# Optimization experiments

Measured on AMD Instinct MI355X. Metric: run time of the kernel, lower is better.

The kernel has to match this reference:

```python
import jax, jax.numpy as jnp
import numpy as np

N = 100_000   # nodes
E = 1_600_000 # edges
G = 128       # graphs in batch
DIN, DOUT = 100, 200


def setup_inputs() -> dict:
    key = jax.random.key(0)
    ks = jax.random.split(key, 12)
    def lin_w(k, fan_in, fan_out):
        return (jax.random.normal(k, (fan_in, fan_out), jnp.float32) / np.sqrt(fan_in)).astype(jnp.float32)
    return {
        "x": jax.random.normal(ks[0], (N, DIN), jnp.float32),
        "edge_index": jax.random.randint(ks[1], (2, E), 0, N, dtype=jnp.int32),
        "batch": jnp.sort(jax.random.randint(ks[2], (N,), 0, G, dtype=jnp.int32)),
        "W1": lin_w(ks[3], DIN, DOUT),  "b1": jnp.zeros((DOUT,), jnp.float32),
        "Wc": lin_w(ks[4], DOUT, DOUT), "bc": jnp.zeros((DOUT,), jnp.float32),
        "W2": lin_w(ks[5], DOUT, DOUT), "b2": jnp.zeros((DOUT,), jnp.float32),
        "W3": lin_w(ks[6], DOUT, DOUT), "b3": jnp.zeros((DOUT,), jnp.float32),
        "Wcls": lin_w(ks[7], DOUT, 2),  "bcls": jnp.zeros((2,), jnp.float32),
    }


def gcn_conv(x, W, b, src, dst, n_nodes):
    """PyG GCNConv: D^{-1/2}(A+I)D^{-1/2} X W + b, symmetric norm with self-loops."""
    h = x @ W  # [N, Dout]
    # degree at targets including the self-loop (+1)
    deg = jax.ops.segment_sum(jnp.ones((src.shape[0],), x.dtype), dst, num_segments=n_nodes) + 1.0
    dinv = jax.lax.rsqrt(deg)  # [N]
    # gather -> normalize -> scatter-add (messages along edges)
    msg = h[src] * (dinv[src] * dinv[dst])[:, None]          # [E, Dout]
    agg = jax.ops.segment_sum(msg, dst, num_segments=n_nodes)  # [N, Dout]
    # self-loop contribution handled analytically: norm_ii = dinv[i]^2
    agg = agg + h * (dinv * dinv)[:, None]
    return agg + b


def reference(x, edge_index, batch, W1, b1, Wc, bc, W2, b2, W3, b3, Wcls, bcls):
    src, dst = edge_index[0], edge_index[1]
    h = jax.nn.relu(gcn_conv(x, W1, b1, src, dst, N))
    # dropout is identity at eval time
    h = h @ Wc + bc
    h = jax.nn.relu(gcn_conv(h, W2, b2, src, dst, N))
    h = gcn_conv(h, W3, b3, src, dst, N)
    pooled = jax.ops.segment_max(h, batch, num_segments=G)  # global max pool -> [G, Dout]
    logits = pooled @ Wcls + bcls
    return jax.nn.softmax(logits, axis=1)
```

## Files before the change

### kernel.cpp

```cpp
#include <hip/hip_runtime.h>
#include <stdint.h>

#define N_NODES 100000
#define N_EDGES 1600000
#define N_GRAPHS 128
#define DIN 100
#define DOUT 200
#define LDH 200
#define LDX 104

#define NB 98
#define BCAP 18432
#define EPB 8192

typedef unsigned short u16;
typedef unsigned int u32;
typedef _Float16 f16;
typedef f16 half8 __attribute__((ext_vector_type(8)));
typedef f16 half4 __attribute__((ext_vector_type(4)));
typedef f16 half2v __attribute__((ext_vector_type(2)));
typedef float floatx4 __attribute__((ext_vector_type(4)));

__device__ __forceinline__ float h2f(u16 h) {
  f16 x; __builtin_memcpy(&x, &h, 2); return (float)x;
}
__device__ __forceinline__ u16 f2h(float f) {
  f16 x = (f16)f; u16 r; __builtin_memcpy(&r, &x, 2); return r;
}
__device__ __forceinline__ float u2f(u32 u) {
  float f; __builtin_memcpy(&f, &u, 4); return f;
}

__device__ __forceinline__ void pack_frag(const float* __restrict__ W, int K, int nfrag,
                                          u16* __restrict__ out, int idx) {
  if (idx >= nfrag) return;
  int lane = idx & 63;
  int t = idx >> 6;
  int ct = t % 13, ks = t / 13;
  int n = ct * 16 + (lane & 15);
  int kbase = ks * 32 + (lane >> 4) * 8;
  u16 v[8];
  #pragma unroll
  for (int j = 0; j < 8; ++j) {
    int k = kbase + j;
    float f = (k < K && n < DOUT) ? W[(size_t)k * DOUT + n] : 0.f;
    v[j] = f2h(f);
  }
  uint4 o;
  o.x = (u32)v[0] | ((u32)v[1] << 16);
  o.y = (u32)v[2] | ((u32)v[3] << 16);
  o.z = (u32)v[4] | ((u32)v[5] << 16);
  o.w = (u32)v[6] | ((u32)v[7] << 16);
  *(uint4*)(out + (size_t)idx * 8) = o;
}

#define B_X2H   25000
#define B_GB    25391
#define B_COMB  25549
#define B_PK1   25562
#define B_PK3   25585
#define B_TOT   25586
__global__ void k_prep(const float* __restrict__ x, u16* __restrict__ xh,
                       const int* __restrict__ batch, int* __restrict__ gstart,
                       int* __restrict__ gend, int* __restrict__ gcur,
                       const float* __restrict__ Wc, const float* __restrict__ bc,
                       const float* __restrict__ W2, float* __restrict__ Wc2,
                       float* __restrict__ bc2, const float* __restrict__ W1,
                       const float* __restrict__ W3, u16* __restrict__ Wpk1,
                       u16* __restrict__ Wpk3) {
  int b = blockIdx.x, t = threadIdx.x;
  if (b < B_X2H) {
    int gid = b * 256 + t;
    int node = gid >> 6, lane = gid & 63;
    if (node >= N_NODES) return;
    if (lane >= 50) {
      if (lane < 52) {
        int c = 100 + (lane - 50) * 2;
        *(half2v*)(xh + (size_t)node * LDX + c) = half2v{0, 0};
      }
      return;
    }
    float2 v = *(const float2*)(x + (size_t)node * DIN + lane * 2);
    half2v o; o[0] = (f16)v.x; o[1] = (f16)v.y;
    *(half2v*)(xh + (size_t)node * LDX + lane * 2) = o;
  } else if (b < B_GB) {
    int i = (b - B_X2H) * 256 + t;
    if (i >= N_NODES) return;
    int g = batch[i];
    if (i == 0 || batch[i - 1] != g) gstart[g] = i;
    if (i == N_NODES - 1 || batch[i + 1] != g) gend[g] = i;
  } else if (b < B_COMB) {
    int gid = (b - B_GB) * 256 + t;
    if (gid >= 201 * DOUT) return;
    int r = gid / DOUT, c = gid % DOUT;
    const float* a = (r < DOUT) ? (Wc + (size_t)r * DOUT) : bc;
    float s = 0.f;
    for (int k = 0; k < DOUT; ++k) s += a[k] * W2[(size_t)k * DOUT + c];
    if (r < DOUT) Wc2[(size_t)r * DOUT + c] = s;
    else bc2[c] = s;
  } else if (b < B_PK1) {
    pack_frag(W1, DIN, 4 * 13 * 64, Wpk1, (b - B_COMB) * 256 + t);
  } else if (b < B_PK3) {
    pack_frag(W3, DOUT, 7 * 13 * 64, Wpk3, (b - B_PK1) * 256 + t);
  } else {
    if (t < NB) gcur[t] = 0;
  }
}

__global__ void k_bucket(const int* __restrict__ src, const int* __restrict__ dst,
                         int* __restrict__ gcur, uint2* __restrict__ ebuf, int E) {
  __shared__ int hist[NB];
  __shared__ int base[NB];
  __shared__ int cur[NB];
  int t = threadIdx.x;
  int e0 = blockIdx.x * EPB;
  int e1 = min(e0 + EPB, E);
  if (t < NB) { hist[t] = 0; cur[t] = 0; }
  __syncthreads();
  for (int i = e0 + t; i < e1; i += 256)
    atomicAdd(&hist[dst[i] >> 10], 1);
  __syncthreads();
  if (t < NB) base[t] = atomicAdd(&gcur[t], hist[t]);
  __syncthreads();
  for (int i = e0 + t; i < e1; i += 256) {
    int d = dst[i];
    int b = d >> 10;
    int off = atomicAdd(&cur[b], 1);
    int pos = base[b] + off;
    if (pos < BCAP)
      ebuf[(size_t)b * BCAP + pos] = make_uint2((u32)d, (u32)src[i]);
  }
}

__global__ void k_csr(const uint2* __restrict__ ebuf, const int* __restrict__ gcur,
                      int* __restrict__ rowptr, float* __restrict__ dinv,
                      int* __restrict__ colv) {
  __shared__ int s_cnt[1024];
  __shared__ int s_cur[1024];
  __shared__ int s_scan[256];
  __shared__ int s_g[NB];
  __shared__ int s_base;
  int b = blockIdx.x, t = threadIdx.x;
  if (t < NB) s_g[t] = gcur[t];
  for (int j = t; j < 1024; j += 256) s_cnt[j] = 0;
  __syncthreads();
  if (t == 0) {
    int run = 0;
    for (int i = 0; i < b; ++i) run += s_g[i];
    s_base = run;
    if (b == NB - 1) rowptr[N_NODES] = run + s_g[b];
  }
  __syncthreads();
  int cnt = s_g[b];
  int base = s_base;
  int node0 = b << 10;
  int nlim = N_NODES - node0; if (nlim > 1024) nlim = 1024;
  const uint2* eb = ebuf + (size_t)b * BCAP;
  for (int i = t; i < cnt; i += 256)
    atomicAdd(&s_cnt[eb[i].x & 1023], 1);
  __syncthreads();
  int v0 = s_cnt[4 * t + 0], v1 = s_cnt[4 * t + 1];
  int v2 = s_cnt[4 * t + 2], v3 = s_cnt[4 * t + 3];
  int s = v0 + v1 + v2 + v3;
  s_scan[t] = s;
  __syncthreads();
  for (int o = 1; o < 256; o <<= 1) {
    int x = (t >= o) ? s_scan[t - o] : 0;
    __syncthreads();
    s_scan[t] += x;
    __syncthreads();
  }
  int run = s_scan[t] - s;
  int vv[4] = {v0, v1, v2, v3};
  #pragma unroll
  for (int j = 0; j < 4; ++j) {
    int jj = 4 * t + j;
    s_cur[jj] = base + run;
    if (jj < nlim) {
      rowptr[node0 + jj] = base + run;
      dinv[node0 + jj] = rsqrtf((float)vv[j] + 1.0f);
    }
    run += vv[j];
  }
  __syncthreads();
  for (int i = t; i < cnt; i += 256) {
    uint2 e = eb[i];
    int pos = atomicAdd(&s_cur[e.x & 1023], 1);
    colv[pos] = (int)e.y;
  }
}

#define P_FUSE 6250
#define P_TOT  6273
__global__ void k_post(const int* __restrict__ col, const float* __restrict__ dinv,
                       uint2* __restrict__ colw, const float* __restrict__ Wc2,
                       u16* __restrict__ Wpk2) {
  int b = blockIdx.x, t = threadIdx.x;
  if (b < P_FUSE) {
    int i = b * 256 + t;
    if (i < N_EDGES) {
      int s = col[i];
      float w = dinv[s];
      u32 wu; __builtin_memcpy(&wu, &w, 4);
      colw[i] = make_uint2((u32)s, wu);
    }
  } else {
    pack_frag(Wc2, DOUT, 7 * 13 * 64, Wpk2, (b - P_FUSE) * 256 + t);
  }
}

template <int NKS>
__global__ __launch_bounds__(256) void k_gemm_mfma(const u16* __restrict__ A, int lda,
                                                   const u16* __restrict__ Wpk,
                                                   const float* __restrict__ bias,
                                                   u16* __restrict__ C, int relu, int nrows) {
  int wv = threadIdx.x >> 6;
  int lane = threadIdx.x & 63;
  int r0 = blockIdx.x * 128 + wv * 32;
  int m = lane & 15, q = lane >> 4;
  int row0 = r0 + m, row1 = r0 + 16 + m;
  bool ok0 = (row0 < nrows), ok1 = (row1 < nrows);
  const u16* a0p = A + (size_t)row0 * lda + q * 8;
  const u16* a1p = A + (size_t)row1 * lda + q * 8;

  floatx4 acc0[13], acc1[13];
  #pragma unroll
  for (int ct = 0; ct < 13; ++ct) {
    acc0[ct] = floatx4{0.f, 0.f, 0.f, 0.f};
    acc1[ct] = floatx4{0.f, 0.f, 0.f, 0.f};
  }

  const u16* wp = Wpk + (size_t)lane * 8;
  #pragma unroll
  for (int ks = 0; ks < NKS; ++ks) {
    half8 a0 = ok0 ? *(const half8*)(a0p + ks * 32) : half8{0, 0, 0, 0, 0, 0, 0, 0};
    half8 a1 = ok1 ? *(const half8*)(a1p + ks * 32) : half8{0, 0, 0, 0, 0, 0, 0, 0};
    #pragma unroll
    for (int ct = 0; ct < 13; ++ct) {
      half8 bfr = *(const half8*)(wp + (size_t)(ks * 13 + ct) * 512);
      acc0[ct] = __builtin_amdgcn_mfma_f32_16x16x32_f16(a0, bfr, acc0[ct], 0, 0, 0);
      acc1[ct] = __builtin_amdgcn_mfma_f32_16x16x32_f16(a1, bfr, acc1[ct], 0, 0, 0);
    }
  }

  #pragma unroll
  for (int ct = 0; ct < 13; ++ct) {
    int c = ct * 16 + m;
    if (c >= DOUT) continue;
    float bv = bias ? bias[c] : 0.f;
    #pragma unroll
    for (int rg = 0; rg < 4; ++rg) {
      int or0 = r0 + q * 4 + rg;
      if (or0 < nrows) {
        float v = acc0[ct][rg] + bv;
        if (relu) v = fmaxf(v, 0.f);
        C[(size_t)or0 * LDH + c] = f2h(v);
      }
      int or1 = r0 + 16 + q * 4 + rg;
      if (or1 < nrows) {
        float v = acc1[ct][rg] + bv;
        if (relu) v = fmaxf(v, 0.f);
        C[(size_t)or1 * LDH + c] = f2h(v);
      }
    }
  }
}

__global__ void k_agg200h(const u16* __restrict__ T, const float* __restrict__ dinv,
                          const int* __restrict__ rowptr, const uint2* __restrict__ colw,
                          const float* __restrict__ bias, u16* __restrict__ OUT,
                          int relu) {
  int wave = (blockIdx.x * blockDim.x + threadIdx.x) >> 6;
  int lane = threadIdx.x & 63;
  if (wave >= N_NODES || lane >= 50) return;
  int node = wave;
  int c4 = lane * 4;
  float ax = 0.f, ay = 0.f, az = 0.f, aw = 0.f;
  int beg = rowptr[node], end = rowptr[node + 1];
  int e = beg;
  for (; e + 8 <= end; e += 8) {
    uint2 cw[8];
    half4 tv[8];
    #pragma unroll
    for (int j = 0; j < 8; ++j) cw[j] = colw[e + j];
    #pragma unroll
    for (int j = 0; j < 8; ++j)
      tv[j] = *(const half4*)(T + (size_t)cw[j].x * LDH + c4);
    #pragma unroll
    for (int j = 0; j < 8; ++j) {
      float w = u2f(cw[j].y);
      ax += w * (float)tv[j][0];
      ay += w * (float)tv[j][1];
      az += w * (float)tv[j][2];
      aw += w * (float)tv[j][3];
    }
  }
  for (; e < end; ++e) {
    uint2 cw = colw[e];
    float w = u2f(cw.y);
    half4 tv = *(const half4*)(T + (size_t)cw.x * LDH + c4);
    ax += w * (float)tv[0]; ay += w * (float)tv[1];
    az += w * (float)tv[2]; aw += w * (float)tv[3];
  }
  float di = dinv[node];
  float dii = di * di;
  half4 sv = *(const half4*)(T + (size_t)node * LDH + c4);
  float rx = di * ax + dii * (float)sv[0];
  float ry = di * ay + dii * (float)sv[1];
  float rz = di * az + dii * (float)sv[2];
  float rw = di * aw + dii * (float)sv[3];
  if (bias) {
    rx += bias[c4 + 0]; ry += bias[c4 + 1];
    rz += bias[c4 + 2]; rw += bias[c4 + 3];
  }
  if (relu) {
    rx = fmaxf(rx, 0.f); ry = fmaxf(ry, 0.f);
    rz = fmaxf(rz, 0.f); rw = fmaxf(rw, 0.f);
  }
  half4 o;
  o[0] = (f16)rx; o[1] = (f16)ry; o[2] = (f16)rz; o[3] = (f16)rw;
  *(half4*)(OUT + (size_t)node * LDH + c4) = o;
}

__global__ void k_agg100h(const u16* __restrict__ T, const float* __restrict__ dinv,
                          const int* __restrict__ rowptr, const uint2* __restrict__ colw,
                          u16* __restrict__ OUT) {
  int wave = (blockIdx.x * blockDim.x + threadIdx.x) >> 6;
  int lane = threadIdx.x & 63;
  if (wave >= N_NODES) return;
  int node = wave;
  if (lane >= 50) {
    if (lane < 52) {
      int c = 100 + (lane - 50) * 2;
      *(half2v*)(OUT + (size_t)node * LDX + c) = half2v{0, 0};
    }
    return;
  }
  int c2 = lane * 2;
  float ax = 0.f, ay = 0.f;
  int beg = rowptr[node], end = rowptr[node + 1];
  int e = beg;
  for (; e + 8 <= end; e += 8) {
    uint2 cw[8];
    half2v tv[8];
    #pragma unroll
    for (int j = 0; j < 8; ++j) cw[j] = colw[e + j];
    #pragma unroll
    for (int j = 0; j < 8; ++j)
      tv[j] = *(const half2v*)(T + (size_t)cw[j].x * LDX + c2);
    #pragma unroll
    for (int j = 0; j < 8; ++j) {
      float w = u2f(cw[j].y);
      ax += w * (float)tv[j][0];
      ay += w * (float)tv[j][1];
    }
  }
  for (; e < end; ++e) {
    uint2 cw = colw[e];
    float w = u2f(cw.y);
    half2v tv = *(const half2v*)(T + (size_t)cw.x * LDX + c2);
    ax += w * (float)tv[0]; ay += w * (float)tv[1];
  }
  float di = dinv[node];
  float dii = di * di;
  half2v sv = *(const half2v*)(T + (size_t)node * LDX + c2);
  half2v o;
  o[0] = (f16)(di * ax + dii * (float)sv[0]);
  o[1] = (f16)(di * ay + dii * (float)sv[1]);
  *(half2v*)(OUT + (size_t)node * LDX + c2) = o;
}

#define POOL_CHUNKS 8
__global__ void k_pool1h(const u16* __restrict__ H, const int* __restrict__ gstart,
                         const int* __restrict__ gend, float* __restrict__ part) {
  int g = blockIdx.x, c = blockIdx.y, t = threadIdx.x;
  if (t >= DOUT) return;
  int s = gstart[g], e = gend[g];
  float m = -3.4e38f;
  if (s >= 0 && e >= s && e < N_NODES) {
    int len = e - s + 1;
    int cs = s + (int)(((long long)len * c) / POOL_CHUNKS);
    int ce = s + (int)(((long long)len * (c + 1)) / POOL_CHUNKS);
    for (int i = cs; i < ce; ++i) m = fmaxf(m, h2f(H[(size_t)i * LDH + t]));
  }
  part[(size_t)(g * POOL_CHUNKS + c) * DOUT + t] = m;
}

__global__ void k_poolcls(const float* __restrict__ part, const float* __restrict__ Wcls,
                          const float* __restrict__ bcls, float* __restrict__ out) {
  __shared__ float l0s[256], l1s[256];
  int g = blockIdx.x, t = threadIdx.x;
  float c0 = 0.f, c1 = 0.f;
  if (t < DOUT) {
    float m = -3.4e38f;
    #pragma unroll
    for (int c = 0; c < POOL_CHUNKS; ++c)
      m = fmaxf(m, part[(size_t)(g * POOL_CHUNKS + c) * DOUT + t]);
    c0 = m * Wcls[t * 2 + 0];
    c1 = m * Wcls[t * 2 + 1];
  }
  l0s[t] = c0; l1s[t] = c1;
  __syncthreads();
  for (int o = 128; o > 0; o >>= 1) {
    if (t < o) { l0s[t] += l0s[t + o]; l1s[t] += l1s[t + o]; }
    __syncthreads();
  }
  if (t == 0) {
    float l0 = l0s[0] + bcls[0], l1 = l1s[0] + bcls[1];
    float m = fmaxf(l0, l1);
    float e0 = expf(l0 - m), e1 = expf(l1 - m);
    float inv = 1.0f / (e0 + e1);
    out[g * 2 + 0] = e0 * inv;
    out[g * 2 + 1] = e1 * inv;
  }
}

static inline size_t align256(size_t x) { return (x + 255) & ~(size_t)255; }

extern "C" void kernel_launch(void* const* d_in, const int* in_sizes, int n_in,
                              void* d_out, int out_size, void* d_ws, size_t ws_size,
                              hipStream_t stream) {
  const float* x     = (const float*)d_in[0];
  const int*   ei    = (const int*)d_in[1];
  const int*   batch = (const int*)d_in[2];
  const float* W1    = (const float*)d_in[3];
  const float* b1    = (const float*)d_in[4];
  const float* Wc    = (const float*)d_in[5];
  const float* bc    = (const float*)d_in[6];
  const float* W2    = (const float*)d_in[7];
  const float* b2    = (const float*)d_in[8];
  const float* W3    = (const float*)d_in[9];
  const float* b3    = (const float*)d_in[10];
  const float* Wcls  = (const float*)d_in[11];
  const float* bcls  = (const float*)d_in[12];
  float* out = (float*)d_out;

  const int N = N_NODES, E = N_EDGES;
  const int* src = ei;
  const int* dst = ei + E;

  char* ws = (char*)d_ws;
  size_t off = 0;
  float* dinv   = (float*)(ws + off); off = align256(off + (size_t)N * 4);
  int*   rowptr = (int*)  (ws + off); off = align256(off + (size_t)(N + 1) * 4);
  int*   col    = (int*)  (ws + off); off = align256(off + (size_t)E * 4);
  uint2* colw   = (uint2*)(ws + off); off = align256(off + (size_t)E * 8);
  int*   gcur   = (int*)  (ws + off); off = align256(off + (size_t)NB * 4);
  int*   gstart = (int*)  (ws + off); off = align256(off + 512);
  int*   gend   = (int*)  (ws + off); off = align256(off + 512);
  float* Wc2    = (float*)(ws + off); off = align256(off + (size_t)DOUT * DOUT * 4);
  float* bc2    = (float*)(ws + off); off = align256(off + (size_t)DOUT * 4);
  u16*   Wpk1   = (u16*)  (ws + off); off = align256(off + (size_t)4 * 13 * 64 * 8 * 2);
  u16*   Wpk2   = (u16*)  (ws + off); off = align256(off + (size_t)7 * 13 * 64 * 8 * 2);
  u16*   Wpk3   = (u16*)  (ws + off); off = align256(off + (size_t)7 * 13 * 64 * 8 * 2);
  u16*   xh     = (u16*)  (ws + off); off = align256(off + ((size_t)N * LDX + 128) * 2);
  u16*   bufX   = (u16*)  (ws + off); off = align256(off + ((size_t)N * LDX + 128) * 2);
  u16*   buf0   = (u16*)  (ws + off); off = align256(off + ((size_t)N * LDH + 128) * 2);
  u16*   buf1   = (u16*)  (ws + off); off = align256(off + ((size_t)N * LDH + 128) * 2);
  u16*   buf2   = (u16*)  (ws + off); off = align256(off + ((size_t)N * LDH + 128) * 2);

  uint2* ebuf = (uint2*)buf0;
  float* part = (float*)buf1;

  k_prep<<<B_TOT, 256, 0, stream>>>(x, xh, batch, gstart, gend, gcur,
                                    Wc, bc, W2, Wc2, bc2, W1, W3, Wpk1, Wpk3);
  k_bucket<<<(E + EPB - 1) / EPB, 256, 0, stream>>>(src, dst, gcur, ebuf, E);
  k_csr<<<NB, 256, 0, stream>>>(ebuf, gcur, rowptr, dinv, col);
  k_post<<<P_TOT, 256, 0, stream>>>(col, dinv, colw, Wc2, Wpk2);

  int gemmb = (N + 127) / 128;
  int aggb  = (N + 3) / 4;

  k_agg100h<<<aggb, 256, 0, stream>>>(xh, dinv, rowptr, colw, bufX);
  k_gemm_mfma<4><<<gemmb, 256, 0, stream>>>(bufX, LDX, Wpk1, b1, buf0, 1, N);
  k_gemm_mfma<7><<<gemmb, 256, 0, stream>>>(buf0, LDH, Wpk2, bc2, buf2, 0, N);
  k_agg200h<<<aggb, 256, 0, stream>>>(buf2, dinv, rowptr, colw, b2, buf0, 1);
  k_gemm_mfma<7><<<gemmb, 256, 0, stream>>>(buf0, LDH, Wpk3, nullptr, buf1, 0, N);
  k_agg200h<<<aggb, 256, 0, stream>>>(buf1, dinv, rowptr, colw, b3, buf2, 0);

  dim3 pg(N_GRAPHS, POOL_CHUNKS);
  k_pool1h<<<pg, 256, 0, stream>>>(buf2, gstart, gend, part);
  k_poolcls<<<N_GRAPHS, 256, 0, stream>>>(part, Wcls, bcls, out);
}
```

Before: 720.2 us.

## Fold source-side degree scaling into producers and drop per-edge weight array

```diff
diff --git a/kernel.cpp b/kernel.cpp
--- a/kernel.cpp
+++ b/kernel.cpp
@@ -7,11 +7,11 @@
 #define DIN 100
 #define DOUT 200
 #define LDH 200
-#define LDX 104
-
-#define NB 98
-#define BCAP 18432
-#define EPB 8192
+#define LDX 128
+
+#define NB 391
+#define BCAP 5120
+#define EPB 2048
 
 typedef unsigned short u16;
 typedef unsigned int u32;
@@ -26,9 +26,6 @@
 }
 __device__ __forceinline__ u16 f2h(float f) {
   f16 x = (f16)f; u16 r; __builtin_memcpy(&r, &x, 2); return r;
-}
-__device__ __forceinline__ float u2f(u32 u) {
-  float f; __builtin_memcpy(&f, &u, 4); return f;
 }
 
 __device__ __forceinline__ void pack_frag(const float* __restrict__ W, int K, int nfrag,
@@ -54,14 +51,12 @@
   *(uint4*)(out + (size_t)idx * 8) = o;
 }
 
-#define B_X2H   25000
-#define B_GB    25391
-#define B_COMB  25549
-#define B_PK1   25562
-#define B_PK3   25585
-#define B_TOT   25586
-__global__ void k_prep(const float* __restrict__ x, u16* __restrict__ xh,
-                       const int* __restrict__ batch, int* __restrict__ gstart,
+#define B_GB    391
+#define B_COMB  549
+#define B_PK1   562
+#define B_PK3   585
+#define B_TOT   587
+__global__ void k_prep(const int* __restrict__ batch, int* __restrict__ gstart,
                        int* __restrict__ gend, int* __restrict__ gcur,
                        const float* __restrict__ Wc, const float* __restrict__ bc,
                        const float* __restrict__ W2, float* __restrict__ Wc2,
@@ -69,22 +64,8 @@
                        const float* __restrict__ W3, u16* __restrict__ Wpk1,
                        u16* __restrict__ Wpk3) {
   int b = blockIdx.x, t = threadIdx.x;
-  if (b < B_X2H) {
-    int gid = b * 256 + t;
-    int node = gid >> 6, lane = gid & 63;
-    if (node >= N_NODES) return;
-    if (lane >= 50) {
-      if (lane < 52) {
-        int c = 100 + (lane - 50) * 2;
-        *(half2v*)(xh + (size_t)node * LDX + c) = half2v{0, 0};
-      }
-      return;
-    }
-    float2 v = *(const float2*)(x + (size_t)node * DIN + lane * 2);
-    half2v o; o[0] = (f16)v.x; o[1] = (f16)v.y;
-    *(half2v*)(xh + (size_t)node * LDX + lane * 2) = o;
-  } else if (b < B_GB) {
-    int i = (b - B_X2H) * 256 + t;
+  if (b < B_GB) {
+    int i = b * 256 + t;
     if (i >= N_NODES) return;
     int g = batch[i];
     if (i == 0 || batch[i - 1] != g) gstart[g] = i;
@@ -103,7 +84,8 @@
   } else if (b < B_PK3) {
     pack_frag(W3, DOUT, 7 * 13 * 64, Wpk3, (b - B_PK1) * 256 + t);
   } else {
-    if (t < NB) gcur[t] = 0;
+    int i = (b - B_PK3) * 256 + t;
+    if (i < NB) gcur[i] = 0;
   }
 }
 
@@ -115,16 +97,17 @@
   int t = threadIdx.x;
   int e0 = blockIdx.x * EPB;
   int e1 = min(e0 + EPB, E);
-  if (t < NB) { hist[t] = 0; cur[t] = 0; }
+  for (int j = t; j < NB; j += 256) { hist[j] = 0; cur[j] = 0; }
   __syncthreads();
   for (int i = e0 + t; i < e1; i += 256)
-    atomicAdd(&hist[dst[i] >> 10], 1);
-  __syncthreads();
-  if (t < NB) base[t] = atomicAdd(&gcur[t], hist[t]);
+    atomicAdd(&hist[dst[i] >> 8], 1);
+  __syncthreads();
+  for (int j = t; j < NB; j += 256)
+    base[j] = hist[j] ? atomicAdd(&gcur[j], hist[j]) : 0;
   __syncthreads();
   for (int i = e0 + t; i < e1; i += 256) {
     int d = dst[i];
-    int b = d >> 10;
+    int b = d >> 8;
     int off = atomicAdd(&cur[b], 1);
     int pos = base[b] + off;
     if (pos < BCAP)
@@ -135,14 +118,14 @@
 __global__ void k_csr(const uint2* __restrict__ ebuf, const int* __restrict__ gcur,
                       int* __restrict__ rowptr, float* __restrict__ dinv,
                       int* __restrict__ colv) {
-  __shared__ int s_cnt[1024];
-  __shared__ int s_cur[1024];
+  __shared__ int s_cnt[256];
+  __shared__ int s_cur[256];
   __shared__ int s_scan[256];
   __shared__ int s_g[NB];
   __shared__ int s_base;
   int b = blockIdx.x, t = threadIdx.x;
-  if (t < NB) s_g[t] = gcur[t];
-  for (int j = t; j < 1024; j += 256) s_cnt[j] = 0;
+  for (int j = t; j < NB; j += 256) s_g[j] = gcur[j];
+  s_cnt[t] = 0;
   __syncthreads();
   if (t == 0) {
     int run = 0;
@@ -153,16 +136,13 @@
   __syncthreads();
   int cnt = s_g[b];
   int base = s_base;
-  int node0 = b << 10;
-  int nlim = N_NODES - node0; if (nlim > 1024) nlim = 1024;
+  int node0 = b << 8;
   const uint2* eb = ebuf + (size_t)b * BCAP;
   for (int i = t; i < cnt; i += 256)
-    atomicAdd(&s_cnt[eb[i].x & 1023], 1);
-  __syncthreads();
-  int v0 = s_cnt[4 * t + 0], v1 = s_cnt[4 * t + 1];
-  int v2 = s_cnt[4 * t + 2], v3 = s_cnt[4 * t + 3];
-  int s = v0 + v1 + v2 + v3;
-  s_scan[t] = s;
+    atomicAdd(&s_cnt[eb[i].x & 255], 1);
+  __syncthreads();
+  int v = s_cnt[t];
+  s_scan[t] = v;
   __syncthreads();
   for (int o = 1; o < 256; o <<= 1) {
     int x = (t >= o) ? s_scan[t - o] : 0;
@@ -170,42 +150,42 @@
     s_scan[t] += x;
     __syncthreads();
   }
-  int run = s_scan[t] - s;
-  int vv[4] = {v0, v1, v2, v3};
-  #pragma unroll
-  for (int j = 0; j < 4; ++j) {
-    int jj = 4 * t + j;
-    s_cur[jj] = base + run;
-    if (jj < nlim) {
-      rowptr[node0 + jj] = base + run;
-      dinv[node0 + jj] = rsqrtf((float)vv[j] + 1.0f);
-    }
-    run += vv[j];
+  int run = s_scan[t] - v;
+  s_cur[t] = base + run;
+  int node = node0 + t;
+  if (node < N_NODES) {
+    rowptr[node] = base + run;
+    dinv[node] = rsqrtf((float)v + 1.0f);
   }
   __syncthreads();
   for (int i = t; i < cnt; i += 256) {
     uint2 e = eb[i];
-    int pos = atomicAdd(&s_cur[e.x & 1023], 1);
+    int pos = atomicAdd(&s_cur[e.x & 255], 1);
     colv[pos] = (int)e.y;
   }
 }
 
-#define P_FUSE 6250
-#define P_TOT  6273
-__global__ void k_post(const int* __restrict__ col, const float* __restrict__ dinv,
-                       uint2* __restrict__ colw, const float* __restrict__ Wc2,
+#define P_XS  25000
+#define P_TOT 25023
+__global__ void k_post(const float* __restrict__ x, const float* __restrict__ dinv,
+                       u16* __restrict__ xs, const float* __restrict__ Wc2,
                        u16* __restrict__ Wpk2) {
   int b = blockIdx.x, t = threadIdx.x;
-  if (b < P_FUSE) {
-    int i = b * 256 + t;
-    if (i < N_EDGES) {
-      int s = col[i];
-      float w = dinv[s];
-      u32 wu; __builtin_memcpy(&wu, &w, 4);
-      colw[i] = make_uint2((u32)s, wu);
+  if (b < P_XS) {
+    int gid = b * 256 + t;
+    int node = gid >> 6, lane = gid & 63;
+    if (node >= N_NODES) return;
+    if (lane >= 50) {
+      int c = 100 + (lane - 50) * 2;
+      *(half2v*)(xs + (size_t)node * LDX + c) = half2v{0, 0};
+      return;
     }
+    float d = dinv[node];
+    float2 vv = *(const float2*)(x + (size_t)node * DIN + lane * 2);
+    half2v o; o[0] = (f16)(d * vv.x); o[1] = (f16)(d * vv.y);
+    *(half2v*)(xs + (size_t)node * LDX + lane * 2) = o;
   } else {
-    pack_frag(Wc2, DOUT, 7 * 13 * 64, Wpk2, (b - P_FUSE) * 256 + t);
+    pack_frag(Wc2, DOUT, 7 * 13 * 64, Wpk2, (b - P_XS) * 256 + t);
   }
 }
 
@@ -213,6 +193,7 @@
 __global__ __launch_bounds__(256) void k_gemm_mfma(const u16* __restrict__ A, int lda,
                                                    const u16* __restrict__ Wpk,
                                                    const float* __restrict__ bias,
+                                                   const float* __restrict__ rowscale,
                                                    u16* __restrict__ C, int relu, int nrows) {
   int wv = threadIdx.x >> 6;
   int lane = threadIdx.x & 63;
@@ -243,6 +224,15 @@
     }
   }
 
+  float sc0[4], sc1[4];
+  #pragma unroll
+  for (int rg = 0; rg < 4; ++rg) {
+    int or0 = r0 + q * 4 + rg;
+    int or1 = r0 + 16 + q * 4 + rg;
+    sc0[rg] = (rowscale && or0 < nrows) ? rowscale[or0] : 1.f;
+    sc1[rg] = (rowscale && or1 < nrows) ? rowscale[or1] : 1.f;
+  }
+
   #pragma unroll
   for (int ct = 0; ct < 13; ++ct) {
     int c = ct * 16 + m;
@@ -254,20 +244,20 @@
       if (or0 < nrows) {
         float v = acc0[ct][rg] + bv;
         if (relu) v = fmaxf(v, 0.f);
-        C[(size_t)or0 * LDH + c] = f2h(v);
+        C[(size_t)or0 * LDH + c] = f2h(v * sc0[rg]);
       }
       int or1 = r0 + 16 + q * 4 + rg;
       if (or1 < nrows) {
         float v = acc1[ct][rg] + bv;
         if (relu) v = fmaxf(v, 0.f);
-        C[(size_t)or1 * LDH + c] = f2h(v);
+        C[(size_t)or1 * LDH + c] = f2h(v * sc1[rg]);
       }
     }
   }
 }
 
 __global__ void k_agg200h(const u16* __restrict__ T, const float* __restrict__ dinv,
-                          const int* __restrict__ rowptr, const uint2* __restrict__ colw,
+                          const int* __restrict__ rowptr, const int* __restrict__ col,
                           const float* __restrict__ bias, u16* __restrict__ OUT,
                           int relu) {
   int wave = (blockIdx.x * blockDim.x + threadIdx.x) >> 6;
@@ -279,36 +269,32 @@
   int beg = rowptr[node], end = rowptr[node + 1];
   int e = beg;
   for (; e + 8 <= end; e += 8) {
-    uint2 cw[8];
+    int s[8];
     half4 tv[8];
     #pragma unroll
-    for (int j = 0; j < 8; ++j) cw[j] = colw[e + j];
+    for (int j = 0; j < 8; ++j) s[j] = col[e + j];
     #pragma unroll
     for (int j = 0; j < 8; ++j)
-      tv[j] = *(const half4*)(T + (size_t)cw[j].x * LDH + c4);
+      tv[j] = *(const half4*)(T + (size_t)s[j] * LDH + c4);
     #pragma unroll
     for (int j = 0; j < 8; ++j) {
-      float w = u2f(cw[j].y);
-      ax += w * (float)tv[j][0];
-      ay += w * (float)tv[j][1];
-      az += w * (float)tv[j][2];
-      aw += w * (float)tv[j][3];
+      ax += (float)tv[j][0];
+      ay += (float)tv[j][1];
+      az += (float)tv[j][2];
+      aw += (float)tv[j][3];
     }
   }
   for (; e < end; ++e) {
-    uint2 cw = colw[e];
-    float w = u2f(cw.y);
-    half4 tv = *(const half4*)(T + (size_t)cw.x * LDH + c4);
-    ax += w * (float)tv[0]; ay += w * (float)tv[1];
-    az += w * (float)tv[2]; aw += w * (float)tv[3];
+    half4 tv = *(const half4*)(T + (size_t)col[e] * LDH + c4);
+    ax += (float)tv[0]; ay += (float)tv[1];
+    az += (float)tv[2]; aw += (float)tv[3];
   }
   float di = dinv[node];
-  float dii = di * di;
   half4 sv = *(const half4*)(T + (size_t)node * LDH + c4);
-  float rx = di * ax + dii * (float)sv[0];
-  float ry = di * ay + dii * (float)sv[1];
-  float rz = di * az + dii * (float)sv[2];
-  float rw = di * aw + dii * (float)sv[3];
+  float rx = di * (ax + (float)sv[0]);
+  float ry = di * (ay + (float)sv[1]);
+  float rz = di * (az + (float)sv[2]);
+  float rw = di * (aw + (float)sv[3]);
   if (bias) {
     rx += bias[c4 + 0]; ry += bias[c4 + 1];
     rz += bias[c4 + 2]; rw += bias[c4 + 3];
@@ -323,17 +309,15 @@
 }
 
 __global__ void k_agg100h(const u16* __restrict__ T, const float* __restrict__ dinv,
-                          const int* __restrict__ rowptr, const uint2* __restrict__ colw,
+                          const int* __restrict__ rowptr, const int* __restrict__ col,
                           u16* __restrict__ OUT) {
   int wave = (blockIdx.x * blockDim.x + threadIdx.x) >> 6;
   int lane = threadIdx.x & 63;
   if (wave >= N_NODES) return;
   int node = wave;
   if (lane >= 50) {
-    if (lane < 52) {
-      int c = 100 + (lane - 50) * 2;
-      *(half2v*)(OUT + (size_t)node * LDX + c) = half2v{0, 0};
-    }
+    int c = 100 + (lane - 50) * 2;
+    *(half2v*)(OUT + (size_t)node * LDX + c) = half2v{0, 0};
     return;
   }
   int c2 = lane * 2;
@@ -341,32 +325,28 @@
   int beg = rowptr[node], end = rowptr[node + 1];
   int e = beg;
   for (; e + 8 <= end; e += 8) {
-    uint2 cw[8];
+    int s[8];
     half2v tv[8];
     #pragma unroll
-    for (int j = 0; j < 8; ++j) cw[j] = colw[e + j];
+    for (int j = 0; j < 8; ++j) s[j] = col[e + j];
     #pragma unroll
     for (int j = 0; j < 8; ++j)
-      tv[j] = *(const half2v*)(T + (size_t)cw[j].x * LDX + c2);
+      tv[j] = *(const half2v*)(T + (size_t)s[j] * LDX + c2);
     #pragma unroll
     for (int j = 0; j < 8; ++j) {
-      float w = u2f(cw[j].y);
-      ax += w * (float)tv[j][0];
-      ay += w * (float)tv[j][1];
+      ax += (float)tv[j][0];
+      ay += (float)tv[j][1];
     }
   }
   for (; e < end; ++e) {
-    uint2 cw = colw[e];
-    float w = u2f(cw.y);
-    half2v tv = *(const half2v*)(T + (size_t)cw.x * LDX + c2);
-    ax += w * (float)tv[0]; ay += w * (float)tv[1];
+    half2v tv = *(const half2v*)(T + (size_t)col[e] * LDX + c2);
+    ax += (float)tv[0]; ay += (float)tv[1];
   }
   float di = dinv[node];
-  float dii = di * di;
   half2v sv = *(const half2v*)(T + (size_t)node * LDX + c2);
   half2v o;
-  o[0] = (f16)(di * ax + dii * (float)sv[0]);
-  o[1] = (f16)(di * ay + dii * (float)sv[1]);
+  o[0] = (f16)(di * (ax + (float)sv[0]));
+  o[1] = (f16)(di * (ay + (float)sv[1]));
   *(half2v*)(OUT + (size_t)node * LDX + c2) = o;
 }
 
@@ -444,7 +424,6 @@
   float* dinv   = (float*)(ws + off); off = align256(off + (size_t)N * 4);
   int*   rowptr = (int*)  (ws + off); off = align256(off + (size_t)(N + 1) * 4);
   int*   col    = (int*)  (ws + off); off = align256(off + (size_t)E * 4);
-  uint2* colw   = (uint2*)(ws + off); off = align256(off + (size_t)E * 8);
   int*   gcur   = (int*)  (ws + off); off = align256(off + (size_t)NB * 4);
   int*   gstart = (int*)  (ws + off); off = align256(off + 512);
   int*   gend   = (int*)  (ws + off); off = align256(off + 512);
@@ -453,7 +432,7 @@
   u16*   Wpk1   = (u16*)  (ws + off); off = align256(off + (size_t)4 * 13 * 64 * 8 * 2);
   u16*   Wpk2   = (u16*)  (ws + off); off = align256(off + (size_t)7 * 13 * 64 * 8 * 2);
   u16*   Wpk3   = (u16*)  (ws + off); off = align256(off + (size_t)7 * 13 * 64 * 8 * 2);
-  u16*   xh     = (u16*)  (ws + off); off = align256(off + ((size_t)N * LDX + 128) * 2);
+  u16*   xs     = (u16*)  (ws + off); off = align256(off + ((size_t)N * LDX + 128) * 2);
   u16*   bufX   = (u16*)  (ws + off); off = align256(off + ((size_t)N * LDX + 128) * 2);
   u16*   buf0   = (u16*)  (ws + off); off = align256(off + ((size_t)N * LDH + 128) * 2);
   u16*   buf1   = (u16*)  (ws + off); off = align256(off + ((size_t)N * LDH + 128) * 2);
@@ -462,21 +441,21 @@
   uint2* ebuf = (uint2*)buf0;
   float* part = (float*)buf1;
 
-  k_prep<<<B_TOT, 256, 0, stream>>>(x, xh, batch, gstart, gend, gcur,
+  k_prep<<<B_TOT, 256, 0, stream>>>(batch, gstart, gend, gcur,
                                     Wc, bc, W2, Wc2, bc2, W1, W3, Wpk1, Wpk3);
   k_bucket<<<(E + EPB - 1) / EPB, 256, 0, stream>>>(src, dst, gcur, ebuf, E);
   k_csr<<<NB, 256, 0, stream>>>(ebuf, gcur, rowptr, dinv, col);
-  k_post<<<P_TOT, 256, 0, stream>>>(col, dinv, colw, Wc2, Wpk2);
+  k_post<<<P_TOT, 256, 0, stream>>>(x, dinv, xs, Wc2, Wpk2);
 
   int gemmb = (N + 127) / 128;
   int aggb  = (N + 3) / 4;
 
-  k_agg100h<<<aggb, 256, 0, stream>>>(xh, dinv, rowptr, colw, bufX);
-  k_gemm_mfma<4><<<gemmb, 256, 0, stream>>>(bufX, LDX, Wpk1, b1, buf0, 1, N);
-  k_gemm_mfma<7><<<gemmb, 256, 0, stream>>>(buf0, LDH, Wpk2, bc2, buf2, 0, N);
-  k_agg200h<<<aggb, 256, 0, stream>>>(buf2, dinv, rowptr, colw, b2, buf0, 1);
-  k_gemm_mfma<7><<<gemmb, 256, 0, stream>>>(buf0, LDH, Wpk3, nullptr, buf1, 0, N);
-  k_agg200h<<<aggb, 256, 0, stream>>>(buf1, dinv, rowptr, colw, b3, buf2, 0);
+  k_agg100h<<<aggb, 256, 0, stream>>>(xs, dinv, rowptr, col, bufX);
+  k_gemm_mfma<4><<<gemmb, 256, 0, stream>>>(bufX, LDX, Wpk1, b1, nullptr, buf0, 1, N);
+  k_gemm_mfma<7><<<gemmb, 256, 0, stream>>>(buf0, LDH, Wpk2, bc2, dinv, buf2, 0, N);
+  k_agg200h<<<aggb, 256, 0, stream>>>(buf2, dinv, rowptr, col, b2, buf0, 1);
+  k_gemm_mfma<7><<<gemmb, 256, 0, stream>>>(buf0, LDH, Wpk3, nullptr, dinv, buf1, 0, N);
+  k_agg200h<<<aggb, 256, 0, stream>>>(buf1, dinv, rowptr, col, b3, buf2, 0);
 
   dim3 pg(N_GRAPHS, POOL_CHUNKS);
   k_pool1h<<<pg, 256, 0, stream>>>(buf2, gstart, gend, part);
```

Result: faster. 681.1 us (median of 2 runs) (-5.4%).
